# Performance work log

Hardware: AMD Instinct MI355X
Metric: run time of the kernel (lower is better)

Reference implementation:

```python
import jax, jax.numpy as jnp
import numpy as np

NUM_HEADS = 12

def setup_inputs() -> dict:
    key = jax.random.key(0)
    k1, k2, k3 = jax.random.split(key, 3)
    B, H, W, C = 8, 32, 32, 768
    x = jax.random.normal(k1, (B, H, W, C), dtype=jnp.float32)
    qkv_w = jax.random.normal(k2, (3 * C, C), dtype=jnp.float32) * (C ** -0.5)
    qkv_b = jnp.zeros((3 * C,), dtype=jnp.float32)
    proj_w = jax.random.normal(k3, (C, C), dtype=jnp.float32) * (C ** -0.5)
    proj_b = jnp.zeros((C,), dtype=jnp.float32)
    return {"x": x, "qkv_w": qkv_w, "qkv_b": qkv_b, "proj_w": proj_w, "proj_b": proj_b}

def reference(x, qkv_w, qkv_b, proj_w, proj_b):
    B, H, W, C = x.shape
    N = H * W
    h = NUM_HEADS
    d = C // h
    scale = d ** -0.5
    xf = x.reshape(B, N, C)
    # fused QKV projection: [B,N,3C] -> [3,B,h,N,d]
    qkv = (xf @ qkv_w.T + qkv_b).reshape(B, N, 3, h, d).transpose(2, 0, 3, 1, 4)
    q, k, v = qkv[0], qkv[1], qkv[2]  # rope = Identity
    # scaled dot-product attention
    scores = jnp.einsum('bhnd,bhmd->bhnm', q, k) * scale
    attn = jax.nn.softmax(scores, axis=-1)
    out = jnp.einsum('bhnm,bhmd->bhnd', attn, v)
    out = out.transpose(0, 2, 1, 3).reshape(B, N, C)
    out = out @ proj_w.T + proj_b
    return out.reshape(B, H, W, C)
```

## Files before the change

### kernel.cpp

```cpp
#include <hip/hip_runtime.h>
#include <math.h>

#define AS1 __attribute__((address_space(1)))
#define AS3 __attribute__((address_space(3)))

typedef __attribute__((ext_vector_type(8))) short bf16x8;
typedef __attribute__((ext_vector_type(4))) float f32x4;

__device__ __forceinline__ unsigned short f2bf(float f) {
    union { float f; unsigned int i; } v; v.f = f;
    unsigned int r = v.i + 0x7FFFu + ((v.i >> 16) & 1u);
    return (unsigned short)(r >> 16);
}

__device__ __forceinline__ unsigned int pack2bf(float lo, float hi) {
    union { float f; unsigned int i; } a, b; a.f = lo; b.f = hi;
    return __builtin_amdgcn_perm(b.i + 0x8000u, a.i + 0x8000u, 0x07060302u);
}

#define NTOK 1024
#define CCH  768
#define HD   64
#define QKS  1536

#define N1C (8192 * 768 / 4)
#define N2C (2304 * 768 / 4)
#define N3C (768 * 768 / 4)

__global__ void cvt_all(const float* __restrict__ x, const float* __restrict__ w1,
                        const float* __restrict__ w2,
                        unsigned short* __restrict__ xb, unsigned short* __restrict__ w1b,
                        unsigned short* __restrict__ w2b)
{
    int i = blockIdx.x * blockDim.x + threadIdx.x;
    const float4* s; ushort4* d; int k;
    if (i < N1C)            { s = (const float4*)x;  d = (ushort4*)xb;  k = i; }
    else if (i < N1C + N2C) { s = (const float4*)w1; d = (ushort4*)w1b; k = i - N1C; }
    else if (i < N1C + N2C + N3C) { s = (const float4*)w2; d = (ushort4*)w2b; k = i - N1C - N2C; }
    else return;
    const float4 v = s[k];
    ushort4 o;
    o.x = f2bf(v.x); o.y = f2bf(v.y); o.z = f2bf(v.z); o.w = f2bf(v.w);
    d[k] = o;
}

__global__ __launch_bounds__(256, 4)
void gemm_proj(const unsigned short* __restrict__ A,
               const unsigned short* __restrict__ W,
               const float* __restrict__ bias,
               float* __restrict__ Cmat)
{
    const int N = 768, K = 768;
    __shared__ __align__(16) unsigned short As[2][64 * 32];
    __shared__ __align__(16) unsigned short Bs[2][128 * 32];

    const int tid  = threadIdx.x;
    const int wave = tid >> 6;
    const int lane = tid & 63;
    const int quad = lane >> 4;
    const int l15  = lane & 15;
    const int wr   = wave >> 1;
    const int wc   = wave & 1;

    const int m0 = blockIdx.x * 64;
    const int n0 = blockIdx.y * 128;

    const unsigned short* AgS = A + (size_t)(m0 + wave * 16 + (lane >> 2)) * K + (lane & 3) * 8;
    const int srow = wave * 32 + (lane >> 2);
    const int scol = (lane & 3) * 8;
    const unsigned short* Wg0 = W + (size_t)(n0 + srow) * K + scol;
    const unsigned short* Wg1 = W + (size_t)(n0 + srow + 16) * K + scol;

    const int da  = wave * 512 + lane * 8;
    const int db0 = (wave * 2 + 0) * 512 + lane * 8;
    const int db1 = (wave * 2 + 1) * 512 + lane * 8;

    f32x4 acc[2][4];
#pragma unroll
    for (int i = 0; i < 2; ++i)
#pragma unroll
        for (int j = 0; j < 4; ++j) acc[i][j] = (f32x4){0.f, 0.f, 0.f, 0.f};

    __builtin_amdgcn_global_load_lds((AS1 void*)(AgS), (AS3 void*)(As[0] + da),  16, 0, 0);
    __builtin_amdgcn_global_load_lds((AS1 void*)(Wg0), (AS3 void*)(Bs[0] + db0), 16, 0, 0);
    __builtin_amdgcn_global_load_lds((AS1 void*)(Wg1), (AS3 void*)(Bs[0] + db1), 16, 0, 0);

#pragma unroll 2
    for (int kc = 0; kc < 24; ++kc) {
        const int cur = kc & 1;
        __syncthreads();
        if (kc < 23) {
            const int nk = (kc + 1) * 32;
            __builtin_amdgcn_global_load_lds((AS1 void*)(AgS + nk), (AS3 void*)(As[cur ^ 1] + da),  16, 0, 0);
            __builtin_amdgcn_global_load_lds((AS1 void*)(Wg0 + nk), (AS3 void*)(Bs[cur ^ 1] + db0), 16, 0, 0);
            __builtin_amdgcn_global_load_lds((AS1 void*)(Wg1 + nk), (AS3 void*)(Bs[cur ^ 1] + db1), 16, 0, 0);
        }

        bf16x8 af[2], bfr[4];
#pragma unroll
        for (int i = 0; i < 2; ++i)
            af[i] = *(const bf16x8*)(As[cur] + (wr * 32 + i * 16 + l15) * 32 + quad * 8);
#pragma unroll
        for (int j = 0; j < 4; ++j)
            bfr[j] = *(const bf16x8*)(Bs[cur] + (wc * 64 + j * 16 + l15) * 32 + quad * 8);
#pragma unroll
        for (int i = 0; i < 2; ++i)
#pragma unroll
            for (int j = 0; j < 4; ++j)
                acc[i][j] = __builtin_amdgcn_mfma_f32_16x16x32_bf16(af[i], bfr[j], acc[i][j], 0, 0, 0);
    }

#pragma unroll
    for (int i = 0; i < 2; ++i) {
        const int row = m0 + wr * 32 + i * 16 + quad * 4;
#pragma unroll
        for (int j = 0; j < 4; ++j) {
            const int col = n0 + wc * 64 + j * 16 + l15;
            const float bv = bias[col];
#pragma unroll
            for (int r = 0; r < 4; ++r)
                Cmat[(size_t)(row + r) * N + col] = acc[i][j][r] + bv;
        }
    }
}

__global__ __launch_bounds__(256, 2)
void gemm_qkv(const unsigned short* __restrict__ A,
              const unsigned short* __restrict__ W,
              const float* __restrict__ bias,
              unsigned short* __restrict__ qk,
              unsigned short* __restrict__ vT)
{
    const int N = 2304, K = 768;
    __shared__ __align__(16) unsigned short As[2][128 * 32];
    __shared__ __align__(16) unsigned short Bs[2][128 * 32];

    const int tid  = threadIdx.x;
    const int wave = tid >> 6;
    const int lane = tid & 63;
    const int quad = lane >> 4;
    const int l15  = lane & 15;
    const int wr   = wave >> 1;
    const int wc   = wave & 1;

    const int m0 = blockIdx.x * 128;
    const int n0 = blockIdx.y * 128;

    const int srow = wave * 32 + (lane >> 2);
    const int scol = (lane & 3) * 8;

    const unsigned short* Ag0 = A + (size_t)(m0 + srow) * K + scol;
    const unsigned short* Ag1 = A + (size_t)(m0 + srow + 16) * K + scol;
    const unsigned short* Wg0 = W + (size_t)(n0 + srow) * K + scol;
    const unsigned short* Wg1 = W + (size_t)(n0 + srow + 16) * K + scol;

    const int d0 = (wave * 2 + 0) * 512 + lane * 8;
    const int d1 = (wave * 2 + 1) * 512 + lane * 8;

    f32x4 acc[4][4];
#pragma unroll
    for (int i = 0; i < 4; ++i)
#pragma unroll
        for (int j = 0; j < 4; ++j) acc[i][j] = (f32x4){0.f, 0.f, 0.f, 0.f};

    __builtin_amdgcn_global_load_lds((AS1 void*)(Ag0), (AS3 void*)(As[0] + d0), 16, 0, 0);
    __builtin_amdgcn_global_load_lds((AS1 void*)(Ag1), (AS3 void*)(As[0] + d1), 16, 0, 0);
    __builtin_amdgcn_global_load_lds((AS1 void*)(Wg0), (AS3 void*)(Bs[0] + d0), 16, 0, 0);
    __builtin_amdgcn_global_load_lds((AS1 void*)(Wg1), (AS3 void*)(Bs[0] + d1), 16, 0, 0);

#pragma unroll 2
    for (int kc = 0; kc < 24; ++kc) {
        const int cur = kc & 1;
        __syncthreads();
        if (kc < 23) {
            const int nk = (kc + 1) * 32;
            __builtin_amdgcn_global_load_lds((AS1 void*)(Ag0 + nk), (AS3 void*)(As[cur ^ 1] + d0), 16, 0, 0);
            __builtin_amdgcn_global_load_lds((AS1 void*)(Ag1 + nk), (AS3 void*)(As[cur ^ 1] + d1), 16, 0, 0);
            __builtin_amdgcn_global_load_lds((AS1 void*)(Wg0 + nk), (AS3 void*)(Bs[cur ^ 1] + d0), 16, 0, 0);
            __builtin_amdgcn_global_load_lds((AS1 void*)(Wg1 + nk), (AS3 void*)(Bs[cur ^ 1] + d1), 16, 0, 0);
        }

        bf16x8 af[4], bfr[4];
#pragma unroll
        for (int i = 0; i < 4; ++i)
            af[i] = *(const bf16x8*)(As[cur] + (wr * 64 + i * 16 + l15) * 32 + quad * 8);
#pragma unroll
        for (int j = 0; j < 4; ++j)
            bfr[j] = *(const bf16x8*)(Bs[cur] + (wc * 64 + j * 16 + l15) * 32 + quad * 8);
#pragma unroll
        for (int i = 0; i < 4; ++i)
#pragma unroll
            for (int j = 0; j < 4; ++j)
                acc[i][j] = __builtin_amdgcn_mfma_f32_16x16x32_bf16(af[i], bfr[j], acc[i][j], 0, 0, 0);
    }

    const int colbase = n0 + wc * 64;
    if (colbase < 1536) {
        const float s = (colbase < 768) ? 0.125f : 1.f;
#pragma unroll
        for (int i = 0; i < 4; ++i) {
            const int row = m0 + wr * 64 + i * 16 + quad * 4;
#pragma unroll
            for (int j = 0; j < 4; ++j) {
                const int col = colbase + j * 16 + l15;
                const float bv = bias[col];
#pragma unroll
                for (int r = 0; r < 4; ++r)
                    qk[(size_t)(row + r) * QKS + col] = f2bf((acc[i][j][r] + bv) * s);
            }
        }
    } else {
#pragma unroll
        for (int i = 0; i < 4; ++i) {
            const int m    = m0 + wr * 64 + i * 16 + quad * 4;
            const int b    = m >> 10;
            const int tok  = m & 1023;
            const int tile = tok >> 6;
            const int K0   = tok & 63;
#pragma unroll
            for (int j = 0; j < 4; ++j) {
                const int col = colbase + j * 16 + l15;
                const int c   = col - 1536;
                const int h   = c >> 6, d = c & 63;
                const float bv = bias[col];
                const int bh     = b * 12 + h;
                const int region = (d >> 4) * 2 + (K0 >> 5);
                const int L      = ((K0 >> 3) & 3) * 16 + (d & 15);
                uint2 o;
                o.x = pack2bf(acc[i][j][0] + bv, acc[i][j][1] + bv);
                o.y = pack2bf(acc[i][j][2] + bv, acc[i][j][3] + bv);
                *(uint2*)(vT + (((size_t)(bh * 16 + tile) * 8 + region) << 9) + L * 8 + (K0 & 7)) = o;
            }
        }
    }
}

__global__ __launch_bounds__(256, 4)
void attn_fused(const unsigned short* __restrict__ qk,
                const unsigned short* __restrict__ vT,
                unsigned short* __restrict__ aout)
{
    __shared__ __align__(16) unsigned short Kf[2][8 * 512];
    __shared__ __align__(16) unsigned short Vt[2][8 * 512];
    __shared__ __align__(16) unsigned short Ps[8 * 512];

    const int tid  = threadIdx.x;
    const int wave = tid >> 6;
    const int lane = tid & 63;
    const int quad = lane >> 4;
    const int l15  = lane & 15;

    const int lin = blockIdx.x;
    const int bh  = lin % 96;
    const int qt  = lin / 96;
    const int b   = bh / 12;
    const int h   = bh % 12;

    const unsigned short* Qg  = qk + (size_t)b * NTOK * QKS + (size_t)h * HD;
    const unsigned short* Kg  = Qg + CCH;
    const unsigned short* vTb = vT + (size_t)bh * 16 * 8 * 512;

    const int q0 = qt * 128;

    bf16x8 qf[2][2];
#pragma unroll
    for (int qb = 0; qb < 2; ++qb)
#pragma unroll
        for (int ks = 0; ks < 2; ++ks)
            qf[qb][ks] = *(const bf16x8*)(Qg + (size_t)(q0 + wave * 32 + qb * 16 + l15) * QKS
                                              + ks * 32 + quad * 8);

    f32x4 oacc[2][4];
#pragma unroll
    for (int qb = 0; qb < 2; ++qb)
#pragma unroll
        for (int nb = 0; nb < 4; ++nb) oacc[qb][nb] = (f32x4){0.f, 0.f, 0.f, 0.f};
    float lrow[2] = {0.f, 0.f};

    const unsigned short* kdma = Kg + (size_t)(wave * 16 + l15) * QKS + quad * 8;

#pragma unroll
    for (int ks = 0; ks < 2; ++ks)
        __builtin_amdgcn_global_load_lds((AS1 void*)(kdma + ks * 32),
            (AS3 void*)(Kf[0] + (wave * 2 + ks) * 512 + lane * 8), 16, 0, 0);
#pragma unroll
    for (int u = 0; u < 2; ++u)
        __builtin_amdgcn_global_load_lds((AS1 void*)(vTb + (size_t)(wave * 2 + u) * 512 + lane * 8),
            (AS3 void*)(Vt[0] + (wave * 2 + u) * 512 + lane * 8), 16, 0, 0);

    for (int t = 0; t < 16; ++t) {
        const int cur = t & 1;
        __syncthreads();

        if (t < 15) {
            const int nxt = cur ^ 1;
#pragma unroll
            for (int ks = 0; ks < 2; ++ks)
                __builtin_amdgcn_global_load_lds((AS1 void*)(kdma + (size_t)((t + 1) * 64) * QKS + ks * 32),
                    (AS3 void*)(Kf[nxt] + (wave * 2 + ks) * 512 + lane * 8), 16, 0, 0);
#pragma unroll
            for (int u = 0; u < 2; ++u)
                __builtin_amdgcn_global_load_lds((AS1 void*)(vTb + ((size_t)(t + 1) * 8 + wave * 2 + u) * 512 + lane * 8),
                    (AS3 void*)(Vt[nxt] + (wave * 2 + u) * 512 + lane * 8), 16, 0, 0);
        }

        f32x4 sacc[2][4];
#pragma unroll
        for (int qb = 0; qb < 2; ++qb)
#pragma unroll
            for (int jk = 0; jk < 4; ++jk) sacc[qb][jk] = (f32x4){0.f, 0.f, 0.f, 0.f};
#pragma unroll
        for (int ks = 0; ks < 2; ++ks) {
            bf16x8 kf[4];
#pragma unroll
            for (int jk = 0; jk < 4; ++jk)
                kf[jk] = *(const bf16x8*)(Kf[cur] + (jk * 2 + ks) * 512 + lane * 8);
#pragma unroll
            for (int qb = 0; qb < 2; ++qb)
#pragma unroll
                for (int jk = 0; jk < 4; ++jk)
                    sacc[qb][jk] = __builtin_amdgcn_mfma_f32_16x16x32_bf16(
                        kf[jk], qf[qb][ks], sacc[qb][jk], 0, 0, 0);
        }

#pragma unroll
        for (int qb = 0; qb < 2; ++qb) {
            float rsum = 0.f;
#pragma unroll
            for (int jk = 0; jk < 4; ++jk)
#pragma unroll
                for (int r = 0; r < 4; ++r) {
                    const float p = __expf(sacc[qb][jk][r]);
                    sacc[qb][jk][r] = p;
                    rsum += p;
                }
            rsum += __shfl_xor(rsum, 16);
            rsum += __shfl_xor(rsum, 32);
            lrow[qb] += rsum;
        }

#pragma unroll
        for (int p = 0; p < 2; ++p) {
#pragma unroll
            for (int qb = 0; qb < 2; ++qb)
#pragma unroll
                for (int jh = 0; jh < 2; ++jh) {
                    const int jk = 2 * p + jh;
                    uint2 o;
                    o.x = pack2bf(sacc[qb][jk][0], sacc[qb][jk][1]);
                    o.y = pack2bf(sacc[qb][jk][2], sacc[qb][jk][3]);
                    const int off = (wave * 2 + qb) * 512
                                  + ((jh * 2 + (quad >> 1)) * 16 + l15) * 8 + (quad & 1) * 4;
                    *(uint2*)&Ps[off] = o;
                }
            bf16x8 pf[2], vf[4];
#pragma unroll
            for (int qb = 0; qb < 2; ++qb)
                pf[qb] = *(const bf16x8*)(Ps + (wave * 2 + qb) * 512 + lane * 8);
#pragma unroll
            for (int nb = 0; nb < 4; ++nb)
                vf[nb] = *(const bf16x8*)(Vt[cur] + (nb * 2 + p) * 512 + lane * 8);
#pragma unroll
            for (int qb = 0; qb < 2; ++qb)
#pragma unroll
                for (int nb = 0; nb < 4; ++nb)
                    oacc[qb][nb] = __builtin_amdgcn_mfma_f32_16x16x32_bf16(
                        vf[nb], pf[qb], oacc[qb][nb], 0, 0, 0);
        }
    }

#pragma unroll
    for (int qb = 0; qb < 2; ++qb) {
        const float inv = 1.f / lrow[qb];
        const size_t tok = (size_t)(b * NTOK + q0 + wave * 32 + qb * 16 + l15);
#pragma unroll
        for (int nb = 0; nb < 4; ++nb) {
            uint2 o;
            o.x = pack2bf(oacc[qb][nb][0] * inv, oacc[qb][nb][1] * inv);
            o.y = pack2bf(oacc[qb][nb][2] * inv, oacc[qb][nb][3] * inv);
            *(uint2*)(aout + tok * CCH + h * HD + nb * 16 + quad * 4) = o;
        }
    }
}

extern "C" void kernel_launch(void* const* d_in, const int* in_sizes, int n_in,
                              void* d_out, int out_size, void* d_ws, size_t ws_size,
                              hipStream_t stream)
{
    const float* x      = (const float*)d_in[0];
    const float* qkv_w  = (const float*)d_in[1];
    const float* qkv_b  = (const float*)d_in[2];
    const float* proj_w = (const float*)d_in[3];
    const float* proj_b = (const float*)d_in[4];
    float* out = (float*)d_out;

    unsigned short* qk  = (unsigned short*)d_ws;
    unsigned short* att = qk  + (size_t)8192 * 1536;
    unsigned short* xb  = att + (size_t)8192 * 768;
    unsigned short* wqb = xb  + (size_t)8192 * 768;
    unsigned short* wpb = wqb + (size_t)2304 * 768;
    unsigned short* vT  = wpb + (size_t)768 * 768;

    dim3 blk(256);
    cvt_all<<<dim3((N1C + N2C + N3C + 255) / 256), blk, 0, stream>>>(x, qkv_w, proj_w, xb, wqb, wpb);
    gemm_qkv<<<dim3(64, 18), blk, 0, stream>>>(xb, wqb, qkv_b, qk, vT);
    attn_fused<<<dim3(768), blk, 0, stream>>>(qk, vT, att);
    gemm_proj<<<dim3(128, 6), blk, 0, stream>>>(att, wpb, proj_b, out);
}
```

Measured before the change: 188.7 us.

## Restructure QKV GEMM to 256x256 tiles with triple-buffered swizzled LDS pipeline

The QKV projection GEMM moves from 128x128 tiles with 256 threads and double buffering to 256x256 tiles with 512 threads, triple-buffered LDS staging, an XOR swizzle against bank conflicts, and a grouped block-index remap for L2 locality. Explicit vmcnt waits, raw barriers, sched_barrier and setprio are meant to overlap global-to-LDS loads with MFMA work and cut operand reloads per FLOP. The cost is much more LDS (96KB) and more accumulator registers, which may limit occupancy, and a 288-block grid that can leave CUs unevenly loaded.

```diff
diff --git a/kernel.cpp b/kernel.cpp
--- a/kernel.cpp
+++ b/kernel.cpp
@@ -124,82 +124,106 @@
     }
 }
 
-__global__ __launch_bounds__(256, 2)
+#define QKV_STAGE(t, buf) do {                                                               \
+    __builtin_amdgcn_global_load_lds((AS1 void*)(Ag0 + (t) * 32), (AS3 void*)(As[buf] + dst0), 16, 0, 0); \
+    __builtin_amdgcn_global_load_lds((AS1 void*)(Ag1 + (t) * 32), (AS3 void*)(As[buf] + dst1), 16, 0, 0); \
+    __builtin_amdgcn_global_load_lds((AS1 void*)(Wg0 + (t) * 32), (AS3 void*)(Bs[buf] + dst0), 16, 0, 0); \
+    __builtin_amdgcn_global_load_lds((AS1 void*)(Wg1 + (t) * 32), (AS3 void*)(Bs[buf] + dst1), 16, 0, 0); \
+  } while (0)
+
+#define QKV_STEP(cur) do {                                                                   \
+    bf16x8 af[8], bfv[4];                                                                    \
+    _Pragma("unroll")                                                                        \
+    for (int i = 0; i < 8; ++i)                                                              \
+        af[i] = *(const bf16x8*)((const char*)&As[0][0] + (cur) * 16384 + dA + i * 1024);    \
+    _Pragma("unroll")                                                                        \
+    for (int j = 0; j < 4; ++j)                                                              \
+        bfv[j] = *(const bf16x8*)((const char*)&Bs[0][0] + (cur) * 16384 + dB + j * 1024);   \
+    __builtin_amdgcn_s_setprio(1);                                                           \
+    _Pragma("unroll")                                                                        \
+    for (int i = 0; i < 8; ++i)                                                              \
+      _Pragma("unroll")                                                                      \
+      for (int j = 0; j < 4; ++j)                                                            \
+        acc[i][j] = __builtin_amdgcn_mfma_f32_16x16x32_bf16(af[i], bfv[j], acc[i][j], 0, 0, 0); \
+    __builtin_amdgcn_s_setprio(0);                                                           \
+  } while (0)
+
+__global__ __launch_bounds__(512, 2)
 void gemm_qkv(const unsigned short* __restrict__ A,
               const unsigned short* __restrict__ W,
               const float* __restrict__ bias,
               unsigned short* __restrict__ qk,
               unsigned short* __restrict__ vT)
 {
-    const int N = 2304, K = 768;
-    __shared__ __align__(16) unsigned short As[2][128 * 32];
-    __shared__ __align__(16) unsigned short Bs[2][128 * 32];
+    const int K = 768;
+    __shared__ __align__(16) unsigned short As[3][256 * 32];
+    __shared__ __align__(16) unsigned short Bs[3][256 * 32];
 
     const int tid  = threadIdx.x;
     const int wave = tid >> 6;
     const int lane = tid & 63;
     const int quad = lane >> 4;
     const int l15  = lane & 15;
-    const int wr   = wave >> 1;
-    const int wc   = wave & 1;
-
-    const int m0 = blockIdx.x * 128;
-    const int n0 = blockIdx.y * 128;
-
-    const int srow = wave * 32 + (lane >> 2);
-    const int scol = (lane & 3) * 8;
-
-    const unsigned short* Ag0 = A + (size_t)(m0 + srow) * K + scol;
-    const unsigned short* Ag1 = A + (size_t)(m0 + srow + 16) * K + scol;
-    const unsigned short* Wg0 = W + (size_t)(n0 + srow) * K + scol;
-    const unsigned short* Wg1 = W + (size_t)(n0 + srow + 16) * K + scol;
-
-    const int d0 = (wave * 2 + 0) * 512 + lane * 8;
-    const int d1 = (wave * 2 + 1) * 512 + lane * 8;
-
-    f32x4 acc[4][4];
-#pragma unroll
-    for (int i = 0; i < 4; ++i)
+    const int wr   = wave >> 2;
+    const int wc   = wave & 3;
+
+    const int lin = blockIdx.x;
+    const int idx = (lin & 7) * 36 + (lin >> 3);
+    const int bx  = idx & 31;
+    const int by  = idx >> 5;
+    const int m0  = bx * 256;
+    const int n0  = by * 256;
+
+    const int srow  = tid >> 2;
+    const int scolb = ((tid & 3) << 4)
+                    ^ (((tid >> 3) & 1) << 4)
+                    ^ (((tid >> 4) & 1) << 5);
+    const unsigned short* Ag0 = A + (size_t)(m0 + srow)       * K + (scolb >> 1);
+    const unsigned short* Ag1 = A + (size_t)(m0 + 128 + srow) * K + (scolb >> 1);
+    const unsigned short* Wg0 = W + (size_t)(n0 + srow)       * K + (scolb >> 1);
+    const unsigned short* Wg1 = W + (size_t)(n0 + 128 + srow) * K + (scolb >> 1);
+    const int dst0 = tid * 8;
+    const int dst1 = tid * 8 + 4096;
+
+    int dA = (wr * 128 + l15) * 64 + quad * 16;
+    dA ^= ((dA >> 7) & 1) << 4;  dA ^= ((dA >> 8) & 1) << 5;
+    int dB = (wc * 64 + l15) * 64 + quad * 16;
+    dB ^= ((dB >> 7) & 1) << 4;  dB ^= ((dB >> 8) & 1) << 5;
+
+    f32x4 acc[8][4];
+#pragma unroll
+    for (int i = 0; i < 8; ++i)
 #pragma unroll
         for (int j = 0; j < 4; ++j) acc[i][j] = (f32x4){0.f, 0.f, 0.f, 0.f};
 
-    __builtin_amdgcn_global_load_lds((AS1 void*)(Ag0), (AS3 void*)(As[0] + d0), 16, 0, 0);
-    __builtin_amdgcn_global_load_lds((AS1 void*)(Ag1), (AS3 void*)(As[0] + d1), 16, 0, 0);
-    __builtin_amdgcn_global_load_lds((AS1 void*)(Wg0), (AS3 void*)(Bs[0] + d0), 16, 0, 0);
-    __builtin_amdgcn_global_load_lds((AS1 void*)(Wg1), (AS3 void*)(Bs[0] + d1), 16, 0, 0);
-
-#pragma unroll 2
-    for (int kc = 0; kc < 24; ++kc) {
-        const int cur = kc & 1;
-        __syncthreads();
-        if (kc < 23) {
-            const int nk = (kc + 1) * 32;
-            __builtin_amdgcn_global_load_lds((AS1 void*)(Ag0 + nk), (AS3 void*)(As[cur ^ 1] + d0), 16, 0, 0);
-            __builtin_amdgcn_global_load_lds((AS1 void*)(Ag1 + nk), (AS3 void*)(As[cur ^ 1] + d1), 16, 0, 0);
-            __builtin_amdgcn_global_load_lds((AS1 void*)(Wg0 + nk), (AS3 void*)(Bs[cur ^ 1] + d0), 16, 0, 0);
-            __builtin_amdgcn_global_load_lds((AS1 void*)(Wg1 + nk), (AS3 void*)(Bs[cur ^ 1] + d1), 16, 0, 0);
-        }
-
-        bf16x8 af[4], bfr[4];
-#pragma unroll
-        for (int i = 0; i < 4; ++i)
-            af[i] = *(const bf16x8*)(As[cur] + (wr * 64 + i * 16 + l15) * 32 + quad * 8);
-#pragma unroll
-        for (int j = 0; j < 4; ++j)
-            bfr[j] = *(const bf16x8*)(Bs[cur] + (wc * 64 + j * 16 + l15) * 32 + quad * 8);
-#pragma unroll
-        for (int i = 0; i < 4; ++i)
-#pragma unroll
-            for (int j = 0; j < 4; ++j)
-                acc[i][j] = __builtin_amdgcn_mfma_f32_16x16x32_bf16(af[i], bfr[j], acc[i][j], 0, 0, 0);
-    }
+    QKV_STAGE(0, 0);
+    QKV_STAGE(1, 1);
+    asm volatile("s_waitcnt vmcnt(4)" ::: "memory");
+    __builtin_amdgcn_s_barrier();
+    __builtin_amdgcn_sched_barrier(0);
+
+#pragma unroll
+    for (int t = 0; t < 22; ++t) {
+        const int cur = t % 3;
+        QKV_STAGE(t + 2, (t + 2) % 3);
+        __builtin_amdgcn_sched_barrier(0);
+        QKV_STEP(cur);
+        asm volatile("s_waitcnt vmcnt(4)" ::: "memory");
+        __builtin_amdgcn_s_barrier();
+        __builtin_amdgcn_sched_barrier(0);
+    }
+    QKV_STEP(1);
+    asm volatile("s_waitcnt vmcnt(0)" ::: "memory");
+    __builtin_amdgcn_s_barrier();
+    __builtin_amdgcn_sched_barrier(0);
+    QKV_STEP(2);
 
     const int colbase = n0 + wc * 64;
     if (colbase < 1536) {
         const float s = (colbase < 768) ? 0.125f : 1.f;
 #pragma unroll
-        for (int i = 0; i < 4; ++i) {
-            const int row = m0 + wr * 64 + i * 16 + quad * 4;
+        for (int i = 0; i < 8; ++i) {
+            const int row = m0 + wr * 128 + i * 16 + quad * 4;
 #pragma unroll
             for (int j = 0; j < 4; ++j) {
                 const int col = colbase + j * 16 + l15;
@@ -211,8 +235,8 @@
         }
     } else {
 #pragma unroll
-        for (int i = 0; i < 4; ++i) {
-            const int m    = m0 + wr * 64 + i * 16 + quad * 4;
+        for (int i = 0; i < 8; ++i) {
+            const int m    = m0 + wr * 128 + i * 16 + quad * 4;
             const int b    = m >> 10;
             const int tok  = m & 1023;
             const int tile = tok >> 6;
@@ -401,9 +425,8 @@
     unsigned short* wpb = wqb + (size_t)2304 * 768;
     unsigned short* vT  = wpb + (size_t)768 * 768;
 
-    dim3 blk(256);
-    cvt_all<<<dim3((N1C + N2C + N3C + 255) / 256), blk, 0, stream>>>(x, qkv_w, proj_w, xb, wqb, wpb);
-    gemm_qkv<<<dim3(64, 18), blk, 0, stream>>>(xb, wqb, qkv_b, qk, vT);
-    attn_fused<<<dim3(768), blk, 0, stream>>>(qk, vT, att);
-    gemm_proj<<<dim3(128, 6), blk, 0, stream>>>(att, wpb, proj_b, out);
-}
+    cvt_all<<<dim3((N1C + N2C + N3C + 255) / 256), dim3(256), 0, stream>>>(x, qkv_w, proj_w, xb, wqb, wpb);
+    gemm_qkv<<<dim3(288), dim3(512), 0, stream>>>(xb, wqb, qkv_b, qk, vT);
+    attn_fused<<<dim3(768), dim3(256), 0, stream>>>(qk, vT, att);
+    gemm_proj<<<dim3(128, 6), dim3(256), 0, stream>>>(att, wpb, proj_b, out);
+}
```

Result: slower. 198.9 us (+5.4%).

## Restructure QKV GEMM to keep full weight slab in LDS and stream A from registers

Applied to the files above, without the earlier changes.

The QKV GEMM now uses 512-thread blocks with 256x64 output tiles. Each block loads its entire 64x768 weight slab into LDS once, with an XOR swizzle. A fragments are loaded straight from global memory into registers and prefetched one step ahead, which removes per-k-step barriers and double-buffered LDS staging. A swizzled block-index mapping groups blocks that share weights. In exchange the block uses 96KB of LDS and runs at one block per CU, and A loads are uncoalesced direct global reads whose latency may be exposed.

```diff
diff --git a/kernel.cpp b/kernel.cpp
--- a/kernel.cpp
+++ b/kernel.cpp
@@ -124,85 +124,93 @@
     }
 }
 
-__global__ __launch_bounds__(256, 2)
+__global__ __launch_bounds__(512, 1)
 void gemm_qkv(const unsigned short* __restrict__ A,
               const unsigned short* __restrict__ W,
               const float* __restrict__ bias,
               unsigned short* __restrict__ qk,
               unsigned short* __restrict__ vT)
 {
-    const int N = 2304, K = 768;
-    __shared__ __align__(16) unsigned short As[2][128 * 32];
-    __shared__ __align__(16) unsigned short Bs[2][128 * 32];
+    __shared__ __align__(16) unsigned short Bs[12 * 4096];
 
     const int tid  = threadIdx.x;
     const int wave = tid >> 6;
     const int lane = tid & 63;
     const int quad = lane >> 4;
     const int l15  = lane & 15;
-    const int wr   = wave >> 1;
-    const int wc   = wave & 1;
-
-    const int m0 = blockIdx.x * 128;
-    const int n0 = blockIdx.y * 128;
-
-    const int srow = wave * 32 + (lane >> 2);
-    const int scol = (lane & 3) * 8;
-
-    const unsigned short* Ag0 = A + (size_t)(m0 + srow) * K + scol;
-    const unsigned short* Ag1 = A + (size_t)(m0 + srow + 16) * K + scol;
-    const unsigned short* Wg0 = W + (size_t)(n0 + srow) * K + scol;
-    const unsigned short* Wg1 = W + (size_t)(n0 + srow + 16) * K + scol;
-
-    const int d0 = (wave * 2 + 0) * 512 + lane * 8;
-    const int d1 = (wave * 2 + 1) * 512 + lane * 8;
-
-    f32x4 acc[4][4];
-#pragma unroll
-    for (int i = 0; i < 4; ++i)
+
+    const int lin = blockIdx.x;
+    const int idx = (lin & 7) * 144 + (lin >> 3);
+    const int mt  = idx / 36;
+    const int nt  = idx % 36;
+    const int m0  = mt * 256;
+    const int n0  = nt * 64;
+
+    {
+        const int r  = tid >> 3;
+        const int sp = tid & 7;
+        const int sl = sp ^ (r & 7);
+        const unsigned short* Wg = W + (size_t)(n0 + r) * 768 + sl * 8;
+#pragma unroll
+        for (int c = 0; c < 12; ++c)
+            __builtin_amdgcn_global_load_lds((AS1 void*)(Wg + c * 64),
+                (AS3 void*)(Bs + c * 4096 + tid * 8), 16, 0, 0);
+    }
+
+    const unsigned short* Ag = A + (size_t)(m0 + wave * 32 + l15) * 768 + quad * 8;
+
+    const int s0  = quad ^ (l15 & 7);
+    const int bb0 = l15 * 64 + s0 * 8;
+    const int bb1 = l15 * 64 + (s0 ^ 4) * 8;
+
+    bf16x8 a0[2], a1[2];
+    a0[0] = *(const bf16x8*)(Ag);
+    a0[1] = *(const bf16x8*)(Ag + 12288);
+    a1[0] = *(const bf16x8*)(Ag + 32);
+    a1[1] = *(const bf16x8*)(Ag + 12288 + 32);
+
+    f32x4 acc[2][4];
+#pragma unroll
+    for (int i = 0; i < 2; ++i)
 #pragma unroll
         for (int j = 0; j < 4; ++j) acc[i][j] = (f32x4){0.f, 0.f, 0.f, 0.f};
 
-    __builtin_amdgcn_global_load_lds((AS1 void*)(Ag0), (AS3 void*)(As[0] + d0), 16, 0, 0);
-    __builtin_amdgcn_global_load_lds((AS1 void*)(Ag1), (AS3 void*)(As[0] + d1), 16, 0, 0);
-    __builtin_amdgcn_global_load_lds((AS1 void*)(Wg0), (AS3 void*)(Bs[0] + d0), 16, 0, 0);
-    __builtin_amdgcn_global_load_lds((AS1 void*)(Wg1), (AS3 void*)(Bs[0] + d1), 16, 0, 0);
-
-#pragma unroll 2
-    for (int kc = 0; kc < 24; ++kc) {
-        const int cur = kc & 1;
-        __syncthreads();
-        if (kc < 23) {
-            const int nk = (kc + 1) * 32;
-            __builtin_amdgcn_global_load_lds((AS1 void*)(Ag0 + nk), (AS3 void*)(As[cur ^ 1] + d0), 16, 0, 0);
-            __builtin_amdgcn_global_load_lds((AS1 void*)(Ag1 + nk), (AS3 void*)(As[cur ^ 1] + d1), 16, 0, 0);
-            __builtin_amdgcn_global_load_lds((AS1 void*)(Wg0 + nk), (AS3 void*)(Bs[cur ^ 1] + d0), 16, 0, 0);
-            __builtin_amdgcn_global_load_lds((AS1 void*)(Wg1 + nk), (AS3 void*)(Bs[cur ^ 1] + d1), 16, 0, 0);
-        }
-
-        bf16x8 af[4], bfr[4];
-#pragma unroll
-        for (int i = 0; i < 4; ++i)
-            af[i] = *(const bf16x8*)(As[cur] + (wr * 64 + i * 16 + l15) * 32 + quad * 8);
-#pragma unroll
-        for (int j = 0; j < 4; ++j)
-            bfr[j] = *(const bf16x8*)(Bs[cur] + (wc * 64 + j * 16 + l15) * 32 + quad * 8);
-#pragma unroll
-        for (int i = 0; i < 4; ++i)
-#pragma unroll
-            for (int j = 0; j < 4; ++j)
-                acc[i][j] = __builtin_amdgcn_mfma_f32_16x16x32_bf16(af[i], bfr[j], acc[i][j], 0, 0, 0);
-    }
-
-    const int colbase = n0 + wc * 64;
-    if (colbase < 1536) {
-        const float s = (colbase < 768) ? 0.125f : 1.f;
-#pragma unroll
-        for (int i = 0; i < 4; ++i) {
-            const int row = m0 + wr * 64 + i * 16 + quad * 4;
+    __syncthreads();
+
+#define QKV_SUB(aReg, bb, cIdx, stNext) do {                                   \
+    bf16x8 bF[4];                                                              \
+    _Pragma("unroll")                                                          \
+    for (int j = 0; j < 4; ++j)                                                \
+        bF[j] = *(const bf16x8*)(Bs + (cIdx) * 4096 + j * 1024 + (bb));        \
+    bf16x8 nA0, nA1;                                                           \
+    if ((stNext) < 24) {                                                       \
+        nA0 = *(const bf16x8*)(Ag + (stNext) * 32);                            \
+        nA1 = *(const bf16x8*)(Ag + 12288 + (stNext) * 32);                    \
+    }                                                                          \
+    _Pragma("unroll")                                                          \
+    for (int j = 0; j < 4; ++j)                                                \
+        acc[0][j] = __builtin_amdgcn_mfma_f32_16x16x32_bf16(aReg[0], bF[j], acc[0][j], 0, 0, 0); \
+    _Pragma("unroll")                                                          \
+    for (int j = 0; j < 4; ++j)                                                \
+        acc[1][j] = __builtin_amdgcn_mfma_f32_16x16x32_bf16(aReg[1], bF[j], acc[1][j], 0, 0, 0); \
+    if ((stNext) < 24) { aReg[0] = nA0; aReg[1] = nA1; }                       \
+} while (0)
+
+#pragma unroll
+    for (int s2 = 0; s2 < 12; ++s2) {
+        QKV_SUB(a0, bb0, s2, 2 * s2 + 2);
+        QKV_SUB(a1, bb1, s2, 2 * s2 + 3);
+    }
+#undef QKV_SUB
+
+    if (n0 < 1536) {
+        const float s = (n0 < 768) ? 0.125f : 1.f;
+#pragma unroll
+        for (int i = 0; i < 2; ++i) {
+            const int row = m0 + wave * 32 + i * 16 + quad * 4;
 #pragma unroll
             for (int j = 0; j < 4; ++j) {
-                const int col = colbase + j * 16 + l15;
+                const int col = n0 + j * 16 + l15;
                 const float bv = bias[col];
 #pragma unroll
                 for (int r = 0; r < 4; ++r)
@@ -211,15 +219,15 @@
         }
     } else {
 #pragma unroll
-        for (int i = 0; i < 4; ++i) {
-            const int m    = m0 + wr * 64 + i * 16 + quad * 4;
+        for (int i = 0; i < 2; ++i) {
+            const int m    = m0 + wave * 32 + i * 16 + quad * 4;
             const int b    = m >> 10;
             const int tok  = m & 1023;
             const int tile = tok >> 6;
             const int K0   = tok & 63;
 #pragma unroll
             for (int j = 0; j < 4; ++j) {
-                const int col = colbase + j * 16 + l15;
+                const int col = n0 + j * 16 + l15;
                 const int c   = col - 1536;
                 const int h   = c >> 6, d = c & 63;
                 const float bv = bias[col];
@@ -401,9 +409,8 @@
     unsigned short* wpb = wqb + (size_t)2304 * 768;
     unsigned short* vT  = wpb + (size_t)768 * 768;
 
-    dim3 blk(256);
-    cvt_all<<<dim3((N1C + N2C + N3C + 255) / 256), blk, 0, stream>>>(x, qkv_w, proj_w, xb, wqb, wpb);
-    gemm_qkv<<<dim3(64, 18), blk, 0, stream>>>(xb, wqb, qkv_b, qk, vT);
-    attn_fused<<<dim3(768), blk, 0, stream>>>(qk, vT, att);
-    gemm_proj<<<dim3(128, 6), blk, 0, stream>>>(att, wpb, proj_b, out);
-}
+    cvt_all<<<dim3((N1C + N2C + N3C + 255) / 256), dim3(256), 0, stream>>>(x, qkv_w, proj_w, xb, wqb, wpb);
+    gemm_qkv<<<dim3(1152), dim3(512), 0, stream>>>(xb, wqb, qkv_b, qk, vT);
+    attn_fused<<<dim3(768), dim3(256), 0, stream>>>(qk, vT, att);
+    gemm_proj<<<dim3(128, 6), dim3(256), 0, stream>>>(att, wpb, proj_b, out);
+}
```

Result: slower. 222.1 us (+17.7%).
